# Kernel optimization log

Measured on AMD Instinct MI355X. Metric: run time of the kernel, lower is better.

## Reference

```python
import jax, jax.numpy as jnp
import numpy as np

N_NODES = 100000
N_EDGES = 1600000
IN_DIM, HID_DIM, OUT_DIM = 128, 256, 128


def setup_inputs() -> dict:
    key = jax.random.key(0)
    ks = jax.random.split(key, 5)
    x = jax.random.normal(ks[0], (N_NODES, IN_DIM), dtype=jnp.float32)
    src = jax.random.randint(ks[1], (N_EDGES,), 0, N_NODES, dtype=jnp.int64)
    dst = jax.random.randint(ks[2], (N_EDGES,), 0, N_NODES, dtype=jnp.int64)
    # Glorot-ish init for linear weights (DGL GraphConv default), zero bias
    W1 = jax.random.normal(ks[3], (IN_DIM, HID_DIM), dtype=jnp.float32) * (1.0 / np.sqrt(IN_DIM))
    W2 = jax.random.normal(ks[4], (HID_DIM, OUT_DIM), dtype=jnp.float32) * (1.0 / np.sqrt(HID_DIM))
    b1 = jnp.zeros((HID_DIM,), dtype=jnp.float32)
    b2 = jnp.zeros((OUT_DIM,), dtype=jnp.float32)
    return {"x": x, "src": src, "dst": dst, "W1": W1, "b1": b1, "W2": W2, "b2": b2}


def _degree_norms(src, dst, n_nodes):
    # norm='both': D_out(src)^{-1/2} on messages, D_in(dst)^{-1/2} on aggregate;
    # degrees clamped to min 1 as in DGL.
    ones = jnp.ones(src.shape[0], dtype=jnp.float32)
    deg_out = jax.ops.segment_sum(ones, src, num_segments=n_nodes)
    deg_in = jax.ops.segment_sum(ones, dst, num_segments=n_nodes)
    norm_src = jax.lax.rsqrt(jnp.maximum(deg_out, 1.0))
    norm_dst = jax.lax.rsqrt(jnp.maximum(deg_in, 1.0))
    return norm_src, norm_dst


def _graph_conv(x, src, dst, W, b, norm_src, norm_dst):
    h = x * norm_src[:, None]                                  # [N, d]
    agg = jax.ops.segment_sum(h[src], dst, num_segments=x.shape[0])  # [N, d]
    agg = agg * norm_dst[:, None]
    return agg @ W + b


def reference(x, src, dst, W1, b1, W2, b2):
    norm_src, norm_dst = _degree_norms(src, dst, x.shape[0])
    h = jax.nn.relu(_graph_conv(x, src, dst, W1, b1, norm_src, norm_dst))
    out = _graph_conv(h, src, dst, W2, b2, norm_src, norm_dst)
    return out
```

## Files before the change

### kernel.cpp

```cpp
#include <hip/hip_runtime.h>

constexpr int N_NODES = 100000;
constexpr int N_EDGES = 1600000;
constexpr int DIN = 128, DHID = 256, DOUT = 128;

constexpr int NB = 256;
constexpr int BR = 391;
constexpr int CAP = 8192;
constexpr int NBLK1 = 512;
constexpr int CHUNK = (N_EDGES + NBLK1 - 1) / NBLK1;

typedef __bf16 bf16x8 __attribute__((ext_vector_type(8)));
typedef float f32x4 __attribute__((ext_vector_type(4)));

static __device__ __forceinline__ ushort f2bf(float f) {
    uint u = __float_as_uint(f);
    uint r = (u + 0x7FFFu + ((u >> 16) & 1u)) >> 16;
    return (ushort)r;
}
static __device__ __forceinline__ float bf2f(ushort h) {
    return __uint_as_float(((uint)h) << 16);
}
static __device__ __forceinline__ float bflo(uint w) { return __uint_as_float(w << 16); }
static __device__ __forceinline__ float bfhi(uint w) { return __uint_as_float(w & 0xFFFF0000u); }

__global__ __launch_bounds__(256) void part_kernel(const int* __restrict__ src,
                                                   const int* __restrict__ dst,
                                                   int* __restrict__ curA, int* __restrict__ curB,
                                                   uint2* __restrict__ ppair,
                                                   int* __restrict__ psv, int e,
                                                   const float* __restrict__ W1,
                                                   ushort* __restrict__ Wt1,
                                                   const float* __restrict__ W2,
                                                   ushort* __restrict__ Wt2) {
    const int t = threadIdx.x;
    if (blockIdx.x >= NBLK1) {
        int i = (blockIdx.x - NBLK1) * 256 + t;
        if (i < DIN * DHID) {
            int k = i / DHID, c = i - k * DHID;
            Wt1[(size_t)c * DIN + k] = f2bf(W1[i]);
        } else {
            i -= DIN * DHID;
            int k = i / DOUT, c = i - k * DOUT;
            Wt2[(size_t)c * DHID + k] = f2bf(W2[i]);
        }
        return;
    }
    __shared__ uint2 estage[CHUNK];
    __shared__ int hA[NB], hB[NB], rA[NB], rB[NB], cA[NB], cB[NB];
    const int b0 = blockIdx.x * CHUNK;
    const int cnt = min(e - b0, CHUNK);
    hA[t] = 0; hB[t] = 0; cA[t] = 0; cB[t] = 0;
    __syncthreads();
    for (int i = t; i < cnt; i += 256) {
        int s = src[b0 + i], d = dst[b0 + i];
        estage[i] = make_uint2((uint)d, (uint)s);
        atomicAdd(&hA[d / BR], 1);
        atomicAdd(&hB[s / BR], 1);
    }
    __syncthreads();
    rA[t] = atomicAdd(&curA[t], hA[t]);
    rB[t] = atomicAdd(&curB[t], hB[t]);
    __syncthreads();
    for (int i = t; i < cnt; i += 256) {
        uint2 ed = estage[i];
        int bd = (int)ed.x / BR;
        int bs = (int)ed.y / BR;
        int p = rA[bd] + atomicAdd(&cA[bd], 1);
        if (p < CAP) ppair[(size_t)bd * CAP + p] = ed;
        int q = rB[bs] + atomicAdd(&cB[bs], 1);
        if (q < CAP) psv[(size_t)bs * CAP + q] = (int)ed.y;
    }
}

__global__ __launch_bounds__(512) void csrn_kernel(const int* __restrict__ curA,
                                                   const int* __restrict__ curB,
                                                   const uint2* __restrict__ ppair,
                                                   const int* __restrict__ psv,
                                                   int* __restrict__ csr,
                                                   int* __restrict__ rowstart,
                                                   float* __restrict__ ndst,
                                                   float* __restrict__ nsrc,
                                                   const float* __restrict__ x,
                                                   ushort* __restrict__ xb, int n, int e) {
    __shared__ ushort dloc[CAP];
    __shared__ uint sloc[CAP];
    __shared__ int hist[512], sc[512], exc[512], cur[512];
    __shared__ int sbst;
    const int t = threadIdx.x;
    const int b = blockIdx.x;
    const int first = b * BR;
    const int nr = min(BR, n - first);
    const int cntA = min(curA[b], CAP);
    const size_t base = (size_t)b * CAP;

    if (t < 256) sc[t] = curA[t];
    __syncthreads();
    for (int off = 1; off < 256; off <<= 1) {
        int add = 0;
        if (t < 256 && t >= off) add = sc[t - off];
        __syncthreads();
        if (t < 256) sc[t] += add;
        __syncthreads();
    }
    if (t == 0) {
        sbst = (b == 0) ? 0 : sc[b - 1];
        if (b == 0) rowstart[n] = e;
    }
    hist[t] = 0;
    cur[t] = 0;
    __syncthreads();
    const int bst = sbst;

    for (int i = t; i < cntA; i += 512) {
        uint2 ed = ppair[base + i];
        int dl = (int)ed.x - first;
        dloc[i] = (ushort)dl;
        sloc[i] = ed.y;
        atomicAdd(&hist[dl], 1);
    }
    __syncthreads();
    int h = hist[t];
    sc[t] = h;
    __syncthreads();
    for (int off = 1; off < 512; off <<= 1) {
        int add = (t >= off) ? sc[t - off] : 0;
        __syncthreads();
        sc[t] += add;
        __syncthreads();
    }
    exc[t] = sc[t] - h;
    if (t < nr) {
        rowstart[first + t] = bst + exc[t];
        ndst[first + t] = rsqrtf(fmaxf((float)h, 1.0f));
    }
    __syncthreads();
    for (int i = t; i < cntA; i += 512) {
        int dl = dloc[i];
        int p = exc[dl] + atomicAdd(&cur[dl], 1);
        csr[bst + p] = (int)sloc[i];
    }

    __syncthreads();
    hist[t] = 0;
    __syncthreads();
    const int cntB = min(curB[b], CAP);
    for (int i = t; i < cntB; i += 512) atomicAdd(&hist[psv[base + i] - first], 1);
    __syncthreads();
    float* nsv = (float*)exc;
    if (t < nr) {
        float v = rsqrtf(fmaxf((float)hist[t], 1.0f));
        nsrc[first + t] = v;
        nsv[t] = v;
    }
    __syncthreads();

    const int rl = t >> 5, q = t & 31;
    for (int i = rl; i < nr; i += 16) {
        float s = nsv[i];
        const size_t ro = (size_t)(first + i) * 128;
        float4 v = *(const float4*)&x[ro + q * 4];
        ushort4 o = {f2bf(v.x * s), f2bf(v.y * s), f2bf(v.z * s), f2bf(v.w * s)};
        *(ushort4*)&xb[ro + q * 4] = o;
    }
}

template <bool OUTBF16, bool ADDBIAS>
__global__ __launch_bounds__(256) void aggh_kernel(const ushort* __restrict__ Xb,
                                                   const int* __restrict__ csr,
                                                   const int* __restrict__ rowstart,
                                                   const float* __restrict__ ndst,
                                                   const float* __restrict__ bias,
                                                   float* __restrict__ outf,
                                                   ushort* __restrict__ outb, int n, int half) {
    int g = threadIdx.x >> 3;
    int lane = threadIdx.x & 7;
    int d = blockIdx.x * 32 + g;
    if (d >= n) return;
    int beg = rowstart[d], end = rowstart[d + 1];
    const int fo = half * 64 + lane * 8;
    const ushort* Xp = Xb + fo;
    float acc[8];
#pragma unroll
    for (int j = 0; j < 8; j++) acc[j] = 0.f;

#define ACC8(v)                                   \
    do {                                          \
        acc[0] += bflo(v.x); acc[1] += bfhi(v.x); \
        acc[2] += bflo(v.y); acc[3] += bfhi(v.y); \
        acc[4] += bflo(v.z); acc[5] += bfhi(v.z); \
        acc[6] += bflo(v.w); acc[7] += bfhi(v.w); \
    } while (0)

    int k = beg;
    for (; k + 4 <= end; k += 4) {
        int s0 = csr[k], s1 = csr[k + 1], s2 = csr[k + 2], s3 = csr[k + 3];
        uint4 v0 = *(const uint4*)(Xp + (size_t)s0 * 128);
        uint4 v1 = *(const uint4*)(Xp + (size_t)s1 * 128);
        uint4 v2 = *(const uint4*)(Xp + (size_t)s2 * 128);
        uint4 v3 = *(const uint4*)(Xp + (size_t)s3 * 128);
        ACC8(v0);
        ACC8(v1);
        ACC8(v2);
        ACC8(v3);
    }
    for (; k < end; ++k) {
        uint4 v = *(const uint4*)(Xp + (size_t)csr[k] * 128);
        ACC8(v);
    }
#undef ACC8

    float nd = ndst[d];
#pragma unroll
    for (int j = 0; j < 8; j++) acc[j] *= nd;
    if constexpr (ADDBIAS) {
        float4 b0 = *(const float4*)&bias[fo];
        float4 b1 = *(const float4*)&bias[fo + 4];
        acc[0] += b0.x; acc[1] += b0.y; acc[2] += b0.z; acc[3] += b0.w;
        acc[4] += b1.x; acc[5] += b1.y; acc[6] += b1.z; acc[7] += b1.w;
    }
    if constexpr (OUTBF16) {
        uint4 o;
        o.x = (uint)f2bf(acc[0]) | ((uint)f2bf(acc[1]) << 16);
        o.y = (uint)f2bf(acc[2]) | ((uint)f2bf(acc[3]) << 16);
        o.z = (uint)f2bf(acc[4]) | ((uint)f2bf(acc[5]) << 16);
        o.w = (uint)f2bf(acc[6]) | ((uint)f2bf(acc[7]) << 16);
        *(uint4*)(outb + (size_t)d * 128 + fo) = o;
    } else {
        float4 o0 = {acc[0], acc[1], acc[2], acc[3]};
        float4 o1 = {acc[4], acc[5], acc[6], acc[7]};
        *(float4*)(outf + (size_t)d * 128 + fo) = o0;
        *(float4*)(outf + (size_t)d * 128 + fo + 4) = o1;
    }
}

__global__ __launch_bounds__(256) void fused64_kernel(const ushort* __restrict__ A,
                                                      const ushort* __restrict__ Wt1,
                                                      const float* __restrict__ b1,
                                                      const float* __restrict__ nsrc,
                                                      const ushort* __restrict__ Wt2,
                                                      ushort* __restrict__ T, int M) {
    __shared__ ushort Sa[64][128];
    __shared__ ushort H1[64][128];
    const int row0 = blockIdx.x * 64;
    const int t = threadIdx.x;
    const int w = t >> 6, lane = t & 63;
    const int l16 = lane & 15, lk = lane >> 4;

#pragma unroll
    for (int i = 0; i < 4; i++) {
        int idx = i * 256 + t;
        int r = idx >> 4, oct = idx & 15;
        int gr = row0 + r;
        uint4 v = make_uint4(0u, 0u, 0u, 0u);
        if (gr < M) v = *(const uint4*)&A[(size_t)gr * 128 + oct * 8];
        *(uint4*)((char*)&Sa[0][0] + r * 256 + (oct ^ (r & 15)) * 16) = v;
    }
    __syncthreads();

    f32x4 acc2[4][2];
#pragma unroll
    for (int i = 0; i < 4; i++)
#pragma unroll
        for (int j = 0; j < 2; j++) acc2[i][j] = (f32x4){0.f, 0.f, 0.f, 0.f};

    for (int kh = 0; kh < 2; kh++) {
        f32x4 acc1[2][4];
#pragma unroll
        for (int i = 0; i < 2; i++)
#pragma unroll
            for (int j = 0; j < 4; j++) acc1[i][j] = (f32x4){0.f, 0.f, 0.f, 0.f};

        bf16x8 af[2][4];
#pragma unroll
        for (int i = 0; i < 2; i++)
#pragma unroll
            for (int kb = 0; kb < 4; kb++) {
                int c = w * 32 + i * 16 + l16;
                af[i][kb] =
                    *(const bf16x8*)&Wt1[(size_t)(kh * 128 + c) * 128 + kb * 32 + lk * 8];
            }
#pragma unroll
        for (int kb = 0; kb < 4; kb++) {
            bf16x8 bf_[4];
#pragma unroll
            for (int j = 0; j < 4; j++) {
                int m = j * 16 + l16;
                bf_[j] = *(const bf16x8*)((const char*)&Sa[0][0] + m * 256 +
                                          ((kb * 4 + lk) ^ l16) * 16);
            }
#pragma unroll
            for (int i = 0; i < 2; i++)
#pragma unroll
                for (int j = 0; j < 4; j++)
                    acc1[i][j] =
                        __builtin_amdgcn_mfma_f32_16x16x32_bf16(af[i][kb], bf_[j], acc1[i][j], 0, 0, 0);
        }
        __syncthreads();

#pragma unroll
        for (int i = 0; i < 2; i++) {
            int cb = w * 32 + i * 16 + lk * 4;
            float4 bv = *(const float4*)&b1[kh * 128 + cb];
#pragma unroll
            for (int j = 0; j < 4; j++) {
                int m = j * 16 + l16;
                int gm = row0 + m;
                float ns = nsrc[gm < M ? gm : (M - 1)];
                ushort4 pk;
                pk.x = f2bf(fmaxf(acc1[i][j][0] + bv.x, 0.f) * ns);
                pk.y = f2bf(fmaxf(acc1[i][j][1] + bv.y, 0.f) * ns);
                pk.z = f2bf(fmaxf(acc1[i][j][2] + bv.z, 0.f) * ns);
                pk.w = f2bf(fmaxf(acc1[i][j][3] + bv.w, 0.f) * ns);
                int oct = cb >> 3;
                *(ushort4*)((char*)&H1[0][0] + m * 256 + ((oct ^ l16) & 15) * 16 +
                            (cb & 7) * 2) = pk;
            }
        }
        __syncthreads();

        bf16x8 wb[2][4];
#pragma unroll
        for (int j2 = 0; j2 < 2; j2++)
#pragma unroll
            for (int kb2 = 0; kb2 < 4; kb2++) {
                int c2 = w * 32 + j2 * 16 + l16;
                wb[j2][kb2] =
                    *(const bf16x8*)&Wt2[(size_t)c2 * 256 + kh * 128 + kb2 * 32 + lk * 8];
            }
#pragma unroll
        for (int kb2 = 0; kb2 < 4; kb2++) {
            bf16x8 ha[4];
#pragma unroll
            for (int i2 = 0; i2 < 4; i2++) {
                int m = i2 * 16 + l16;
                ha[i2] = *(const bf16x8*)((const char*)&H1[0][0] + m * 256 +
                                          ((kb2 * 4 + lk) ^ l16) * 16);
            }
#pragma unroll
            for (int i2 = 0; i2 < 4; i2++)
#pragma unroll
                for (int j2 = 0; j2 < 2; j2++)
                    acc2[i2][j2] = __builtin_amdgcn_mfma_f32_16x16x32_bf16(ha[i2], wb[j2][kb2],
                                                                           acc2[i2][j2], 0, 0, 0);
        }
    }

#pragma unroll
    for (int i2 = 0; i2 < 4; i2++) {
#pragma unroll
        for (int j2 = 0; j2 < 2; j2++) {
#pragma unroll
            for (int q = 0; q < 4; q++) {
                int r = row0 + i2 * 16 + lk * 4 + q;
                int c = w * 32 + j2 * 16 + l16;
                if (r < M) T[(size_t)r * DOUT + c] = f2bf(acc2[i2][j2][q]);
            }
        }
    }
}

extern "C" void kernel_launch(void* const* d_in, const int* in_sizes, int n_in,
                              void* d_out, int out_size, void* d_ws, size_t ws_size,
                              hipStream_t stream) {
    const float* x  = (const float*)d_in[0];
    const int*   src = (const int*)d_in[1];
    const int*   dst = (const int*)d_in[2];
    const float* W1 = (const float*)d_in[3];
    const float* b1 = (const float*)d_in[4];
    const float* W2 = (const float*)d_in[5];
    const float* b2 = (const float*)d_in[6];
    float* out = (float*)d_out;

    const int N = N_NODES, E = N_EDGES;

    size_t off = 0;
    auto carve = [&](size_t bytes) -> void* {
        void* p = (char*)d_ws + off;
        off += (bytes + 255) & ~(size_t)255;
        return p;
    };
    int* curA     = (int*)carve(NB * 4);
    int* curB     = (int*)carve(NB * 4);
    int* rowstart = (int*)carve((size_t)(N + 1) * 4);
    float* ndst   = (float*)carve((size_t)N * 4);
    float* nsrc   = (float*)carve((size_t)N * 4);
    int* csr      = (int*)carve((size_t)E * 4);
    ushort* Wt1   = (ushort*)carve(DIN * DHID * 2);
    ushort* Wt2   = (ushort*)carve(DHID * DOUT * 2);
    ushort* xb    = (ushort*)carve((size_t)N * DIN * 2);
    ushort* agg1b = (ushort*)carve((size_t)N * DIN * 2);
    ushort* tb    = (ushort*)carve((size_t)N * DOUT * 2);
    uint2* ppair  = (uint2*)carve((size_t)NB * CAP * 8);
    int*   psv    = (int*)carve((size_t)NB * CAP * 4);

    hipMemsetAsync(curA, 0, 2 * NB * 4, stream);

    part_kernel<<<NBLK1 + 256, 256, 0, stream>>>(src, dst, curA, curB, ppair, psv, E,
                                                 W1, Wt1, W2, Wt2);
    csrn_kernel<<<NB, 512, 0, stream>>>(curA, curB, ppair, psv, csr, rowstart, ndst, nsrc,
                                        x, xb, N, E);

    const int gagg = (N + 31) / 32;
    aggh_kernel<true, false><<<gagg, 256, 0, stream>>>(xb, csr, rowstart, ndst, nullptr,
                                                       nullptr, agg1b, N, 0);
    aggh_kernel<true, false><<<gagg, 256, 0, stream>>>(xb, csr, rowstart, ndst, nullptr,
                                                       nullptr, agg1b, N, 1);

    fused64_kernel<<<(N + 63) / 64, 256, 0, stream>>>(agg1b, Wt1, b1, nsrc, Wt2, tb, N);

    aggh_kernel<false, true><<<gagg, 256, 0, stream>>>(tb, csr, rowstart, ndst, b2,
                                                       out, nullptr, N, 0);
    aggh_kernel<false, true><<<gagg, 256, 0, stream>>>(tb, csr, rowstart, ndst, b2,
                                                       out, nullptr, N, 1);
}
```

Baseline: 233.5 us.

## Pack partition entries compactly and pre-swizzle weights into MFMA fragment order

The partition buffers are compacted. Each dst/src pair now packs the local dst row into the upper 15 bits and the src into the lower 17 bits of one uint, and the src-degree list stores 16-bit local offsets. This halves the scratch traffic between the partition and CSR kernels. The weights are rewritten into MFMA fragment order so each lane in the fused GEMM loads contiguous 16-byte chunks. Both weight fragments are loaded up front, and the bias and nsrc values are hoisted out of the inner loop. The packing assumes node ids fit in 17 bits and local rows in 15 bits, and the hoisted loads raise register pressure.

```diff
diff --git a/kernel.cpp b/kernel.cpp
--- a/kernel.cpp
+++ b/kernel.cpp
@@ -27,22 +27,30 @@
 __global__ __launch_bounds__(256) void part_kernel(const int* __restrict__ src,
                                                    const int* __restrict__ dst,
                                                    int* __restrict__ curA, int* __restrict__ curB,
-                                                   uint2* __restrict__ ppair,
-                                                   int* __restrict__ psv, int e,
+                                                   uint* __restrict__ ppair,
+                                                   ushort* __restrict__ psv, int e,
                                                    const float* __restrict__ W1,
-                                                   ushort* __restrict__ Wt1,
+                                                   ushort* __restrict__ Wf1,
                                                    const float* __restrict__ W2,
-                                                   ushort* __restrict__ Wt2) {
+                                                   ushort* __restrict__ Wf2) {
     const int t = threadIdx.x;
     if (blockIdx.x >= NBLK1) {
         int i = (blockIdx.x - NBLK1) * 256 + t;
         if (i < DIN * DHID) {
-            int k = i / DHID, c = i - k * DHID;
-            Wt1[(size_t)c * DIN + k] = f2bf(W1[i]);
+            int frag = i >> 9, r = i & 511;
+            int lane = r >> 3, ee = r & 7;
+            int kb = frag & 3, ii = (frag >> 2) & 1, w = (frag >> 3) & 3, kh = frag >> 5;
+            int c = w * 32 + ii * 16 + (lane & 15);
+            int k = kb * 32 + (lane >> 4) * 8 + ee;
+            Wf1[i] = f2bf(W1[k * DHID + kh * 128 + c]);
         } else {
-            i -= DIN * DHID;
-            int k = i / DOUT, c = i - k * DOUT;
-            Wt2[(size_t)c * DHID + k] = f2bf(W2[i]);
+            int i2 = i - DIN * DHID;
+            int frag = i2 >> 9, r = i2 & 511;
+            int lane = r >> 3, ee = r & 7;
+            int kb2 = frag & 3, j2 = (frag >> 2) & 1, w = (frag >> 3) & 3, kh = frag >> 5;
+            int c2 = w * 32 + j2 * 16 + (lane & 15);
+            int k2 = kh * 128 + kb2 * 32 + (lane >> 4) * 8 + ee;
+            Wf2[i2] = f2bf(W2[k2 * DOUT + c2]);
         }
         return;
     }
@@ -64,27 +72,27 @@
     __syncthreads();
     for (int i = t; i < cnt; i += 256) {
         uint2 ed = estage[i];
-        int bd = (int)ed.x / BR;
-        int bs = (int)ed.y / BR;
+        int d = (int)ed.x, s = (int)ed.y;
+        int bd = d / BR;
+        int bs = s / BR;
         int p = rA[bd] + atomicAdd(&cA[bd], 1);
-        if (p < CAP) ppair[(size_t)bd * CAP + p] = ed;
+        if (p < CAP) ppair[(size_t)bd * CAP + p] = ((uint)(d - bd * BR) << 17) | (uint)s;
         int q = rB[bs] + atomicAdd(&cB[bs], 1);
-        if (q < CAP) psv[(size_t)bs * CAP + q] = (int)ed.y;
+        if (q < CAP) psv[(size_t)bs * CAP + q] = (ushort)(s - bs * BR);
     }
 }
 
 __global__ __launch_bounds__(512) void csrn_kernel(const int* __restrict__ curA,
                                                    const int* __restrict__ curB,
-                                                   const uint2* __restrict__ ppair,
-                                                   const int* __restrict__ psv,
+                                                   const uint* __restrict__ ppair,
+                                                   const ushort* __restrict__ psv,
                                                    int* __restrict__ csr,
                                                    int* __restrict__ rowstart,
                                                    float* __restrict__ ndst,
                                                    float* __restrict__ nsrc,
                                                    const float* __restrict__ x,
                                                    ushort* __restrict__ xb, int n, int e) {
-    __shared__ ushort dloc[CAP];
-    __shared__ uint sloc[CAP];
+    __shared__ uint ploc[CAP];
     __shared__ int hist[512], sc[512], exc[512], cur[512];
     __shared__ int sbst;
     const int t = threadIdx.x;
@@ -113,11 +121,9 @@
     const int bst = sbst;
 
     for (int i = t; i < cntA; i += 512) {
-        uint2 ed = ppair[base + i];
-        int dl = (int)ed.x - first;
-        dloc[i] = (ushort)dl;
-        sloc[i] = ed.y;
-        atomicAdd(&hist[dl], 1);
+        uint p = ppair[base + i];
+        ploc[i] = p;
+        atomicAdd(&hist[p >> 17], 1);
     }
     __syncthreads();
     int h = hist[t];
@@ -136,16 +142,17 @@
     }
     __syncthreads();
     for (int i = t; i < cntA; i += 512) {
-        int dl = dloc[i];
-        int p = exc[dl] + atomicAdd(&cur[dl], 1);
-        csr[bst + p] = (int)sloc[i];
+        uint p = ploc[i];
+        int dl = p >> 17;
+        int pos = exc[dl] + atomicAdd(&cur[dl], 1);
+        csr[bst + pos] = (int)(p & 0x1FFFFu);
     }
 
     __syncthreads();
     hist[t] = 0;
     __syncthreads();
     const int cntB = min(curB[b], CAP);
-    for (int i = t; i < cntB; i += 512) atomicAdd(&hist[psv[base + i] - first], 1);
+    for (int i = t; i < cntB; i += 512) atomicAdd(&hist[psv[base + i]], 1);
     __syncthreads();
     float* nsv = (float*)exc;
     if (t < nr) {
@@ -235,10 +242,10 @@
 }
 
 __global__ __launch_bounds__(256) void fused64_kernel(const ushort* __restrict__ A,
-                                                      const ushort* __restrict__ Wt1,
+                                                      const ushort* __restrict__ Wf1,
                                                       const float* __restrict__ b1,
                                                       const float* __restrict__ nsrc,
-                                                      const ushort* __restrict__ Wt2,
+                                                      const ushort* __restrict__ Wf2,
                                                       ushort* __restrict__ T, int M) {
     __shared__ ushort Sa[64][128];
     __shared__ ushort H1[64][128];
@@ -247,6 +254,19 @@
     const int w = t >> 6, lane = t & 63;
     const int l16 = lane & 15, lk = lane >> 4;
 
+    float nsv[4];
+#pragma unroll
+    for (int j = 0; j < 4; j++) {
+        int gm = row0 + j * 16 + l16;
+        nsv[j] = nsrc[gm < M ? gm : (M - 1)];
+    }
+    float4 bvv[2][2];
+#pragma unroll
+    for (int kh = 0; kh < 2; kh++)
+#pragma unroll
+        for (int i = 0; i < 2; i++)
+            bvv[kh][i] = *(const float4*)&b1[kh * 128 + w * 32 + i * 16 + lk * 4];
+
 #pragma unroll
     for (int i = 0; i < 4; i++) {
         int idx = i * 256 + t;
@@ -265,21 +285,25 @@
         for (int j = 0; j < 2; j++) acc2[i][j] = (f32x4){0.f, 0.f, 0.f, 0.f};
 
     for (int kh = 0; kh < 2; kh++) {
+        const ushort* w1p = Wf1 + ((size_t)(kh * 4 + w) * 8) * 512 + lane * 8;
+        const ushort* w2p = Wf2 + ((size_t)(kh * 4 + w) * 8) * 512 + lane * 8;
+        bf16x8 af[2][4], wb[2][4];
+#pragma unroll
+        for (int i = 0; i < 2; i++)
+#pragma unroll
+            for (int kb = 0; kb < 4; kb++) af[i][kb] = *(const bf16x8*)(w1p + (i * 4 + kb) * 512);
+#pragma unroll
+        for (int j2 = 0; j2 < 2; j2++)
+#pragma unroll
+            for (int kb2 = 0; kb2 < 4; kb2++)
+                wb[j2][kb2] = *(const bf16x8*)(w2p + (j2 * 4 + kb2) * 512);
+
         f32x4 acc1[2][4];
 #pragma unroll
         for (int i = 0; i < 2; i++)
 #pragma unroll
             for (int j = 0; j < 4; j++) acc1[i][j] = (f32x4){0.f, 0.f, 0.f, 0.f};
 
-        bf16x8 af[2][4];
-#pragma unroll
-        for (int i = 0; i < 2; i++)
-#pragma unroll
-            for (int kb = 0; kb < 4; kb++) {
-                int c = w * 32 + i * 16 + l16;
-                af[i][kb] =
-                    *(const bf16x8*)&Wt1[(size_t)(kh * 128 + c) * 128 + kb * 32 + lk * 8];
-            }
 #pragma unroll
         for (int kb = 0; kb < 4; kb++) {
             bf16x8 bf_[4];
@@ -301,12 +325,11 @@
 #pragma unroll
         for (int i = 0; i < 2; i++) {
             int cb = w * 32 + i * 16 + lk * 4;
-            float4 bv = *(const float4*)&b1[kh * 128 + cb];
+            float4 bv = bvv[kh][i];
 #pragma unroll
             for (int j = 0; j < 4; j++) {
                 int m = j * 16 + l16;
-                int gm = row0 + m;
-                float ns = nsrc[gm < M ? gm : (M - 1)];
+                float ns = nsv[j];
                 ushort4 pk;
                 pk.x = f2bf(fmaxf(acc1[i][j][0] + bv.x, 0.f) * ns);
                 pk.y = f2bf(fmaxf(acc1[i][j][1] + bv.y, 0.f) * ns);
@@ -319,15 +342,6 @@
         }
         __syncthreads();
 
-        bf16x8 wb[2][4];
-#pragma unroll
-        for (int j2 = 0; j2 < 2; j2++)
-#pragma unroll
-            for (int kb2 = 0; kb2 < 4; kb2++) {
-                int c2 = w * 32 + j2 * 16 + l16;
-                wb[j2][kb2] =
-                    *(const bf16x8*)&Wt2[(size_t)c2 * 256 + kh * 128 + kb2 * 32 + lk * 8];
-            }
 #pragma unroll
         for (int kb2 = 0; kb2 < 4; kb2++) {
             bf16x8 ha[4];
@@ -386,18 +400,18 @@
     float* ndst   = (float*)carve((size_t)N * 4);
     float* nsrc   = (float*)carve((size_t)N * 4);
     int* csr      = (int*)carve((size_t)E * 4);
-    ushort* Wt1   = (ushort*)carve(DIN * DHID * 2);
-    ushort* Wt2   = (ushort*)carve(DHID * DOUT * 2);
+    ushort* Wf1   = (ushort*)carve(DIN * DHID * 2);
+    ushort* Wf2   = (ushort*)carve(DHID * DOUT * 2);
     ushort* xb    = (ushort*)carve((size_t)N * DIN * 2);
     ushort* agg1b = (ushort*)carve((size_t)N * DIN * 2);
     ushort* tb    = (ushort*)carve((size_t)N * DOUT * 2);
-    uint2* ppair  = (uint2*)carve((size_t)NB * CAP * 8);
-    int*   psv    = (int*)carve((size_t)NB * CAP * 4);
+    uint*   ppair = (uint*)carve((size_t)NB * CAP * 4);
+    ushort* psv   = (ushort*)carve((size_t)NB * CAP * 2);
 
     hipMemsetAsync(curA, 0, 2 * NB * 4, stream);
 
     part_kernel<<<NBLK1 + 256, 256, 0, stream>>>(src, dst, curA, curB, ppair, psv, E,
-                                                 W1, Wt1, W2, Wt2);
+                                                 W1, Wf1, W2, Wf2);
     csrn_kernel<<<NB, 512, 0, stream>>>(curA, curB, ppair, psv, csr, rowstart, ndst, nsrc,
                                         x, xb, N, E);
 
@@ -407,7 +421,7 @@
     aggh_kernel<true, false><<<gagg, 256, 0, stream>>>(xb, csr, rowstart, ndst, nullptr,
                                                        nullptr, agg1b, N, 1);
 
-    fused64_kernel<<<(N + 63) / 64, 256, 0, stream>>>(agg1b, Wt1, b1, nsrc, Wt2, tb, N);
+    fused64_kernel<<<(N + 63) / 64, 256, 0, stream>>>(agg1b, Wf1, b1, nsrc, Wf2, tb, N);
 
     aggh_kernel<false, true><<<gagg, 256, 0, stream>>>(tb, csr, rowstart, ndst, b2,
                                                        out, nullptr, N, 0);
```

Result: faster. 217.1 us (-7.0%).
